# Optimization experiments

Hardware: AMD Instinct MI355X
Metric: run time of the kernel (lower is better)

Reference implementation:

```python
import jax, jax.numpy as jnp
import numpy as np

B, S, IN_DIM, LATENT, SYM = 16, 256, 512, 512, 128
NUM_NODES, NUM_CODES, MAX_OPS, MAX_BUS = 4, 512, 4, 32
HALT_EPS, MAX_SEQ = 1e-3, 256


def setup_inputs() -> dict:
    key = jax.random.key(0)
    ks = jax.random.split(key, 10)

    def lin(k, out_d, in_d, pre=()):
        kw, kb = jax.random.split(k)
        lim = 1.0 / np.sqrt(in_d).astype(np.float32)
        w = jax.random.uniform(kw, pre + (out_d, in_d), minval=-lim, maxval=lim, dtype=jnp.float32)
        b = jax.random.uniform(kb, pre + (out_d,), minval=-lim, maxval=lim, dtype=jnp.float32)
        return w, b

    x = jax.random.normal(ks[0], (B, S, IN_DIM), jnp.float32)
    ipw, ipb = lin(ks[1], LATENT, IN_DIM)
    tp = jax.random.normal(ks[2], (1, MAX_SEQ, LATENT), jnp.float32)
    N = (NUM_NODES,)
    sw, sb = lin(ks[3], SYM, LATENT, N)
    qw, qb = lin(ks[4], 1, SYM, N)
    rw, rb = lin(ks[5], LATENT, 2 * LATENT, N)
    c1w, c1b = lin(ks[6], LATENT, LATENT + SYM, N)
    c2w, c2b = lin(ks[7], LATENT, LATENT, N)
    cb = jax.random.normal(ks[8], (NUM_NODES, NUM_CODES, SYM), jnp.float32)
    return {"x": x, "input_proj_w": ipw, "input_proj_b": ipb, "token_prompts": tp,
            "sym_w": sw, "sym_b": sb, "qry_w": qw, "qry_b": qb,
            "read_w": rw, "read_b": rb, "c1_w": c1w, "c1_b": c1b,
            "c2_w": c2w, "c2_b": c2b, "codebook": cb}


def _forward(x, input_proj_w, input_proj_b, token_prompts, sym_w, sym_b, qry_w, qry_b,
             read_w, read_b, c1_w, c1_b, c2_w, c2_b, codebook):
    Bx, Sx, _ = x.shape
    N = Bx * Sx
    # input projection + positional prompts
    out = jnp.einsum('bsi,li->bsl', x, input_proj_w) + input_proj_b + token_prompts[:, :Sx, :]
    prev_out = out
    active = jnp.ones((Bx, Sx), bool)
    token_tags = jnp.zeros((Bx, Sx, SYM), x.dtype)
    # TensorBus rolling buffers ([max_bus, B, S, dim]); with default cfg the roll branch never fires
    sym_buf = jnp.zeros((MAX_BUS, Bx, Sx, SYM), x.dtype)          # slot 0 = zero tags (initial append)
    out_buf = jnp.zeros((MAX_BUS, Bx, Sx, LATENT), x.dtype).at[0].set(out)
    msg_mask = jnp.zeros((MAX_BUS,), bool).at[0].set(True)
    ptr = 1  # static python int: appends are a fixed unrolled schedule (1 + MAX_OPS*NUM_NODES <= MAX_BUS)
    slot_ids = jnp.arange(MAX_BUS)

    for t in range(MAX_OPS):
        # snapshot of active messages for this op step (get_active)
        snap_active = msg_mask & (slot_ids < ptr)                  # [MAX_BUS]
        syms_flat = sym_buf.reshape(MAX_BUS, N, SYM)
        outs_flat = out_buf.reshape(MAX_BUS, N, LATENT)
        keep_all = jnp.ones((MAX_BUS,), bool)
        for n in range(NUM_NODES):
            # relevance of each bus message per token; inactive slots masked out of argmax
            rel = jnp.einsum('tnd,d->tn', syms_flat, qry_w[n, 0]) + qry_b[n, 0]
            rel = jnp.where(snap_active[:, None], rel, jnp.asarray(-1e9, rel.dtype))
            top = jnp.argmax(rel, axis=0)                          # [N] chosen message per token
            chosen = jnp.take_along_axis(outs_flat, top[None, :, None], axis=0)[0]  # [N, LATENT]
            bus_ctx = chosen.reshape(Bx, Sx, LATENT)
            z = jnp.concatenate([out, bus_ctx], axis=-1)
            z_read = jnp.einsum('bsk,lk->bsl', z, read_w[n]) + read_b[n]
            raw_sym = jnp.einsum('bsl,dl->bsd', z_read, sym_w[n]) + sym_b[n]
            # EMA quantizer (eval): nearest codebook entry by euclidean distance
            flat = raw_sym.reshape(-1, SYM)
            cbn = codebook[n]
            d2 = (jnp.sum(flat * flat, axis=-1, keepdims=True)
                  - 2.0 * flat @ cbn.T + jnp.sum(cbn * cbn, axis=-1))
            idx = jnp.argmin(d2, axis=-1)
            quant = cbn[idx].reshape(Bx, Sx, SYM)
            h = jnp.concatenate([z_read, quant], axis=-1)
            hid = jax.nn.relu(jnp.einsum('bsk,lk->bsl', h, c1_w[n]) + c1_b[n])
            node_out = jnp.einsum('bsl,ol->bso', hid, c2_w[n]) + c2_b[n] + out
            # halting / selective update
            delta = jnp.linalg.norm(node_out - prev_out, axis=-1)
            halt = (delta < HALT_EPS) & active
            assigned = active if t > 0 else jnp.ones_like(active)
            upd = assigned & jnp.logical_not(halt)
            out = jnp.where(upd[..., None], node_out, out)
            token_tags = jnp.where(upd[..., None], quant, token_tags)
            # bus.append
            sym_buf = sym_buf.at[ptr].set(quant)
            out_buf = out_buf.at[ptr].set(node_out)
            msg_mask = msg_mask.at[ptr].set(True)
            ptr += 1
            # keep_mask: messages never selected by any token stay alive
            counts = jnp.zeros((MAX_BUS,), jnp.int32).at[top].add(1)
            keep_all = keep_all & (counts == 0)
            active = active & jnp.logical_not(halt)
            prev_out = out
        # mark_consumed: ones over valid slots ANDed with per-node keep masks at snapshot-active
        # slots (inactive/new slots get True -> faithful to the torch init_global_mask quirk)
        msg_mask = (slot_ids < ptr) & keep_all
    return out


def reference(x, input_proj_w, input_proj_b, token_prompts, sym_w, sym_b, qry_w, qry_b,
              read_w, read_b, c1_w, c1_b, c2_w, c2_b, codebook):
    return _forward(x, input_proj_w, input_proj_b, token_prompts, sym_w, sym_b, qry_w, qry_b,
                    read_w, read_b, c1_w, c1_b, c2_w, c2_b, codebook)
```

## Files before the change

### kernel.cpp

```cpp
#include <hip/hip_runtime.h>
#include <math.h>

namespace {

typedef _Float16 f16;
typedef __attribute__((ext_vector_type(8))) _Float16 f16x8;
typedef __attribute__((ext_vector_type(4))) float f32x4;

constexpr int TOK = 4096;
constexpr int DL  = 512;
constexpr int DS  = 128;
constexpr int NC  = 512;
constexpr int NSLOT = 13;

__device__ __forceinline__ float wsum(float v){
  #pragma unroll
  for(int o=32;o>0;o>>=1) v += __shfl_xor(v,o);
  return v;
}

__device__ __forceinline__ void gload16(const void* g, void* l){
  __builtin_amdgcn_global_load_lds(
      (const __attribute__((address_space(1))) unsigned int*)g,
      (__attribute__((address_space(3))) unsigned int*)l, 16, 0, 0);
}

__device__ __forceinline__ int slotb(int row, int g){
  return (((row ^ ((row>>2)&1))<<2) | (g ^ (row&3))) << 4;
}

template<int AMODE,int EPI>
__global__ __launch_bounds__(256,2) void mgemm(
    const f16* __restrict__ A1h, const f16* __restrict__ A1l,
    const f16* __restrict__ A2h, const f16* __restrict__ A2l,
    const f16* __restrict__ Bh, const f16* __restrict__ Bl,
    const float* __restrict__ bias, const float* __restrict__ res,
    float* __restrict__ Cf, f16* __restrict__ Ch, f16* __restrict__ Cl,
    f16* __restrict__ C2h, f16* __restrict__ C2l,
    float* __restrict__ scpv, int* __restrict__ scpi, int* __restrict__ idxg,
    const float* __restrict__ relc, const int* __restrict__ msg,
    int* __restrict__ cons, int pt, int node,
    int K, int K0)
{
  constexpr int SMB = 16384;
  __shared__ __align__(16) char smem[4*SMB];
  __shared__ int gsel[64];
  __shared__ float redv[4][32];
  __shared__ int   redi[4][32];
  const int tid = threadIdx.x, w = tid>>6, l = tid&63;
  const int m0 = blockIdx.x*64, n0 = blockIdx.y*64;
  const int NK = K>>5, SW = K0>>5;

  if(AMODE==1){
    if(tid<64){
      int m = m0+tid;
      float best = -1e9f; int bs = 0;
      for(int s=0;s<pt;s++){
        float v = msg[s] ? relc[(size_t)((s<<2)+node)*TOK + m] : -1e9f;
        if(v > best){ best=v; bs=s; }
      }
      gsel[tid]=bs;
      cons[bs]=1;
    }
    __syncthreads();
  }
  if(AMODE==2){
    if(tid<64){
      int m = m0+tid;
      float bv = -INFINITY; int bi = 0;
      #pragma unroll
      for(int y=0;y<8;y++){
        float v = scpv[(size_t)y*TOK + m];
        if(v > bv){ bv=v; bi=scpi[(size_t)y*TOK + m]; }
      }
      gsel[tid]=bi;
      idxg[m]=bi;
    }
    __syncthreads();
  }

  const f16* sp[4]; const f16* sp2[4]; int loff[4];
  #pragma unroll
  for(int i=0;i<4;i++){
    int c = 4*w+i;
    int isA = (c<8);
    int plane = isA ? (c>>2) : ((c-8)>>2);
    int cidx  = isA ? (c&3)  : ((c-8)&3);
    loff[i] = (isA?0:8192) + plane*4096 + cidx*1024;
    int s = (cidx<<6) + l;
    int rp = s>>2, row = rp ^ ((rp>>2)&1), g = (s&3) ^ (row&3);
    int g8 = g<<3;
    if(isA){
      int m = m0 + row;
      const f16* p1 = (plane? A1l : A1h) + ((size_t)m<<9) + g8;
      sp[i] = p1;
      if(AMODE==1)      sp2[i] = (plane? A2l : A2h) + ((size_t)gsel[row]<<21) + ((size_t)m<<9) + g8;
      else if(AMODE==2) sp2[i] = (plane? A2l : A2h) + ((size_t)gsel[row]<<7) + g8;
      else              sp2[i] = p1;
    } else {
      sp[i] = (plane? Bl : Bh) + (size_t)(n0+row)*K + g8;
      sp2[i] = sp[i];
    }
  }

  const int wr = w>>1, wc = w&1, q = l>>4, r = l&15;
  int aoff[2], boff[2];
  #pragma unroll
  for(int i=0;i<2;i++) aoff[i] = slotb(32*wr + 16*i + r, q);
  #pragma unroll
  for(int j=0;j<2;j++) boff[j] = 8192 + slotb(32*wc + 16*j + r, q);

  f32x4 acc1[2][2] = {}, acc2[2][2] = {};

  auto advance = [&](int snext){
    #pragma unroll
    for(int i=0;i<4;i++){
      if(AMODE!=0 && (4*w+i)<8 && snext==SW) sp[i] = sp2[i];
      else                                    sp[i] += 32;
    }
  };
  auto stage = [&](int buf){
    char* dst = smem + buf*SMB;
    #pragma unroll
    for(int i=0;i<4;i++) gload16(sp[i], dst + loff[i]);
  };

  f16x8 X[8], Y[8];
  auto ldfrag = [&](const char* Lb, f16x8* F){
    F[0] = *(const f16x8*)(Lb + aoff[0]);
    F[1] = *(const f16x8*)(Lb + aoff[1]);
    F[2] = *(const f16x8*)(Lb + 4096 + aoff[0]);
    F[3] = *(const f16x8*)(Lb + 4096 + aoff[1]);
    F[4] = *(const f16x8*)(Lb + boff[0]);
    F[5] = *(const f16x8*)(Lb + boff[1]);
    F[6] = *(const f16x8*)(Lb + 4096 + boff[0]);
    F[7] = *(const f16x8*)(Lb + 4096 + boff[1]);
  };
  auto domfma = [&](const f16x8* F){
    #pragma unroll
    for(int i=0;i<2;i++)
      #pragma unroll
      for(int j=0;j<2;j++){
        acc1[i][j] = __builtin_amdgcn_mfma_f32_16x16x32_f16(F[i],   F[4+j], acc1[i][j], 0,0,0);
        acc2[i][j] = __builtin_amdgcn_mfma_f32_16x16x32_f16(F[i],   F[6+j], acc2[i][j], 0,0,0);
        acc2[i][j] = __builtin_amdgcn_mfma_f32_16x16x32_f16(F[2+i], F[4+j], acc2[i][j], 0,0,0);
      }
  };

  stage(0); advance(1);
  stage(1); advance(2);
  stage(2); advance(3);
  asm volatile("s_waitcnt vmcnt(4)" ::: "memory");
  __builtin_amdgcn_s_barrier();
  ldfrag(smem, X);

  for(int kt=0; kt<NK; kt+=2){
    ldfrag(smem + ((kt+1)&3)*SMB, Y);
    if(kt+3 < NK){ stage((kt+3)&3); advance(kt+4); }
    domfma(X);
    if(kt+3 < NK)      { asm volatile("s_waitcnt vmcnt(4)" ::: "memory"); }
    else if(kt+2 < NK) { asm volatile("s_waitcnt vmcnt(0)" ::: "memory"); }
    __builtin_amdgcn_s_barrier();
    if(kt+2 < NK) ldfrag(smem + ((kt+2)&3)*SMB, X);
    if(kt+4 < NK){ stage((kt+4)&3); advance(kt+5); }
    domfma(Y);
    if(kt+4 < NK)      { asm volatile("s_waitcnt vmcnt(4)" ::: "memory"); }
    else if(kt+3 < NK) { asm volatile("s_waitcnt vmcnt(0)" ::: "memory"); }
    if(kt+2 < NK) __builtin_amdgcn_s_barrier();
  }

  if(EPI!=1){
    #pragma unroll
    for(int i=0;i<2;i++)
      #pragma unroll
      for(int j=0;j<2;j++)
        #pragma unroll
        for(int rr=0;rr<4;rr++){
          int rowm = m0 + 32*wr + 16*i + 4*q + rr;
          int coln = n0 + 32*wc + 16*j + r;
          size_t o = ((size_t)rowm<<9) + coln;
          float v = acc1[i][j][rr] + acc2[i][j][rr]*(1.0f/2048.0f) + bias[coln];
          if(EPI==2) v = fmaxf(v, 0.f);
          if(EPI==3) v += res[o];
          if(EPI==4) v += res[(((size_t)(rowm&255))<<9) + coln];
          if(EPI==3 || EPI==4) Cf[o] = v;
          if(EPI==0 || EPI==2 || EPI==4){
            f16 h = (f16)v;
            Ch[o] = h; Cl[o] = (f16)((v-(float)h)*2048.0f);
          }
          if((EPI==3 || EPI==4) && C2h){
            f16 h = (f16)v;
            C2h[o] = h; C2l[o] = (f16)((v-(float)h)*2048.0f);
          }
        }
  } else {
    #pragma unroll
    for(int i=0;i<2;i++)
      #pragma unroll
      for(int rr=0;rr<4;rr++){
        float v0 = acc1[i][0][rr] + acc2[i][0][rr]*(1.0f/2048.0f) + bias[n0+32*wc+r];
        float v1 = acc1[i][1][rr] + acc2[i][1][rr]*(1.0f/2048.0f) + bias[n0+32*wc+16+r];
        float bv; int bc;
        if(v1 > v0){ bv=v1; bc=n0+32*wc+16+r; } else { bv=v0; bc=n0+32*wc+r; }
        #pragma unroll
        for(int o=1;o<16;o<<=1){
          float ov = __shfl_xor(bv,o); int oi = __shfl_xor(bc,o);
          if(ov>bv || (ov==bv && oi<bc)){ bv=ov; bc=oi; }
        }
        if(r==0){ redv[w][16*i+4*q+rr]=bv; redi[w][16*i+4*q+rr]=bc; }
      }
    __syncthreads();
    if(tid<64){
      int wr2 = tid>>5, li = tid&31;
      float bv = redv[2*wr2][li]; int bc = redi[2*wr2][li];
      float ov = redv[2*wr2+1][li]; int oi = redi[2*wr2+1][li];
      if(ov>bv || (ov==bv && oi<bc)){ bv=ov; bc=oi; }
      scpv[(size_t)blockIdx.y*TOK + m0 + tid] = bv;
      scpi[(size_t)blockIdx.y*TOK + m0 + tid] = bc;
    }
  }
}

__global__ void split_k(const float* __restrict__ src, f16* __restrict__ hi,
                        f16* __restrict__ lo, int n){
  for(int i = blockIdx.x*256 + threadIdx.x; i < n; i += gridDim.x*256){
    float v = src[i];
    f16 h = (f16)v;
    hi[i] = h;
    lo[i] = (f16)((v - (float)h)*2048.0f);
  }
}

struct SplitArg { const float* src; f16* hi; f16* lo; int n; };
struct SplitArgs5 { SplitArg a[5]; };
__global__ void splitm_k(SplitArgs5 A){
  int stride = gridDim.x*256;
  #pragma unroll
  for(int s=0;s<5;s++){
    const float* src = A.a[s].src; f16* hi = A.a[s].hi; f16* lo = A.a[s].lo;
    int n = A.a[s].n;
    for(int i = blockIdx.x*256 + threadIdx.x; i < n; i += stride){
      float v = src[i];
      f16 h = (f16)v;
      hi[i] = h;
      lo[i] = (f16)((v - (float)h)*2048.0f);
    }
  }
}

__global__ __launch_bounds__(256)
void wcomb_k(const float* __restrict__ A, const float* __restrict__ Wall,
             float* __restrict__ C)
{
  constexpr int T=256;
  __shared__ float As[32][68];
  __shared__ float Ws[32][132];
  const int tid = threadIdx.x;
  const int m0 = blockIdx.x*64, n0 = blockIdx.y*128;
  const float* W = Wall + (size_t)(m0>>9)*DS*DL;
  const int ty = tid>>4, tx = tid&15;
  float4 pa[2], pw[4];
  auto loadA = [&](int k0){
    #pragma unroll
    for(int it=0; it<2; ++it){
      int v = tid + T*it; int rr = v>>3, c4 = v&7;
      pa[it] = *(const float4*)(A + (size_t)(m0+rr)*DS + k0 + (c4<<2));
    }
  };
  auto loadW = [&](int k0){
    #pragma unroll
    for(int it=0; it<4; ++it){
      int v = tid + T*it; int rr = v>>5, c4 = v&31;
      pw[it] = *(const float4*)(W + (size_t)(k0+rr)*DL + n0 + (c4<<2));
    }
  };
  float acc[4][8];
  #pragma unroll
  for(int i=0;i<4;i++)
    #pragma unroll
    for(int j=0;j<8;j++) acc[i][j]=0.f;
  loadA(0); loadW(0);
  for(int k0=0; k0<DS; k0+=32){
    __syncthreads();
    #pragma unroll
    for(int it=0; it<2; ++it){
      int v = tid + T*it; int rr=v>>3, c4=v&7;
      As[(c4<<2)+0][rr]=pa[it].x; As[(c4<<2)+1][rr]=pa[it].y;
      As[(c4<<2)+2][rr]=pa[it].z; As[(c4<<2)+3][rr]=pa[it].w;
    }
    #pragma unroll
    for(int it=0; it<4; ++it){
      int v = tid + T*it; int rr=v>>5, c4=v&31;
      *(float4*)&Ws[rr][c4<<2] = pw[it];
    }
    __syncthreads();
    if(k0+32 < DS){ loadA(k0+32); loadW(k0+32); }
    #pragma unroll
    for(int kk=0; kk<32; kk++){
      float4 a4 = *(const float4*)&As[kk][ty<<2];
      float4 b0 = *(const float4*)&Ws[kk][tx<<2];
      float4 b1 = *(const float4*)&Ws[kk][64+(tx<<2)];
      float a[4]={a4.x,a4.y,a4.z,a4.w};
      float b[8]={b0.x,b0.y,b0.z,b0.w,b1.x,b1.y,b1.z,b1.w};
      #pragma unroll
      for(int i=0;i<4;i++)
        #pragma unroll
        for(int j=0;j<8;j++) acc[i][j] = fmaf(a[i], b[j], acc[i][j]);
    }
  }
  #pragma unroll
  for(int i=0;i<4;i++){
    int m = m0 + (ty<<2) + i;
    #pragma unroll
    for(int j=0;j<8;j++){
      int n = n0 + ((j<4)? (tx<<2)+j : 64+(tx<<2)+(j-4));
      C[((size_t)m<<9)+n] = acc[i][j];
    }
  }
}

__global__ void init_k(int* __restrict__ msg, int* __restrict__ act,
                       float* __restrict__ relc, const float* __restrict__ qb,
                       int* __restrict__ cons){
  int i = blockIdx.x*256 + threadIdx.x;
  if(i < TOK){
    act[i] = 1;
    #pragma unroll
    for(int nn=0;nn<4;nn++) relc[nn*TOK + i] = qb[nn];
  }
  if(i < 32){ msg[i] = (i==0) ? 1 : 0; cons[i] = 0; }
}

__global__ void bias2_k(const float* __restrict__ cb, const float* __restrict__ sb,
                        float* __restrict__ b2){
  int row = blockIdx.x*4 + (threadIdx.x>>6);
  int lane = threadIdx.x&63;
  const float* cv = cb + ((size_t)row<<7);
  const float* sbn = sb + ((row>>9)<<7);
  float c0=cv[lane], c1=cv[lane+64];
  float nrm = c0*c0 + c1*c1;
  float dt  = c0*sbn[lane] + c1*sbn[lane+64];
  nrm = wsum(nrm); dt = wsum(dt);
  if(lane==0) b2[row] = dt - 0.5f*nrm;
}

__global__ void mupdate_k(const float* __restrict__ no_, float* __restrict__ out,
                          f16* __restrict__ outh, f16* __restrict__ outl,
                          float* __restrict__ relc, const int* __restrict__ idx,
                          const float* __restrict__ cbn, const float* __restrict__ qw,
                          const float* __restrict__ qb, int* __restrict__ act,
                          int* __restrict__ cons, int* __restrict__ msg,
                          int t, int ptr, int pe){
  int m = blockIdx.x*4 + (threadIdx.x>>6);
  int lane = threadIdx.x&63;
  const float* nrow = no_ + ((size_t)m<<9);
  float* orow = out + ((size_t)m<<9);
  float nv[8]; float s=0.f;
  #pragma unroll
  for(int rr=0;rr<8;rr++){
    int c = lane + (rr<<6);
    nv[rr]=nrow[c];
    float d = nv[rr]-orow[c]; s += d*d;
  }
  s = wsum(s);
  float delta = sqrtf(s);
  int a = act[m];
  int halt = (delta < 1e-3f) && a;
  int assigned = (t>0) ? a : 1;
  int upd = assigned && !halt;
  if(lane==0) act[m] = a && !halt;
  if(upd){
    #pragma unroll
    for(int rr=0;rr<8;rr++){
      int c = lane + (rr<<6);
      float v = nv[rr];
      orow[c] = v;
      f16 h = (f16)v;
      outh[((size_t)m<<9)+c] = h;
      outl[((size_t)m<<9)+c] = (f16)((v-(float)h)*2048.0f);
    }
  }
  if(ptr >= 0){
    const float* qv = cbn + ((size_t)idx[m]<<7);
    float q0=qv[lane], q1=qv[lane+64];
    #pragma unroll
    for(int nn=0;nn<4;nn++){
      float pr = q0*qw[(nn<<7)+lane] + q1*qw[(nn<<7)+64+lane];
      pr = wsum(pr);
      if(lane==0) relc[(size_t)((ptr<<2)+nn)*TOK + m] = pr + qb[nn];
    }
  }
  if(pe >= 0 && blockIdx.x==0 && threadIdx.x < 32){
    int s2 = threadIdx.x;
    msg[s2] = (s2 < pe) && !cons[s2];
    cons[s2] = 0;
  }
}

}

extern "C" void kernel_launch(void* const* d_in, const int* in_sizes, int n_in,
                              void* d_out, int out_size, void* d_ws, size_t ws_size,
                              hipStream_t stream)
{
  (void)in_sizes; (void)n_in; (void)out_size; (void)ws_size;
  const float* x   = (const float*)d_in[0];
  const float* ipw = (const float*)d_in[1];
  const float* ipb = (const float*)d_in[2];
  const float* tp  = (const float*)d_in[3];
  const float* sw  = (const float*)d_in[4];
  const float* sb  = (const float*)d_in[5];
  const float* qw  = (const float*)d_in[6];
  const float* qb  = (const float*)d_in[7];
  const float* rw  = (const float*)d_in[8];
  const float* rb  = (const float*)d_in[9];
  const float* c1w = (const float*)d_in[10];
  const float* c1b = (const float*)d_in[11];
  const float* c2w = (const float*)d_in[12];
  const float* c2b = (const float*)d_in[13];
  const float* cb  = (const float*)d_in[14];
  float* out = (float*)d_out;

  char* p = (char*)d_ws;
  auto alloc = [&](size_t b)->char*{ char* r=p; p += (b+255)&~(size_t)255; return r; };
  f16* slabh = (f16*)alloc((size_t)NSLOT*TOK*DL*2);
  f16* slabl = (f16*)alloc((size_t)NSLOT*TOK*DL*2);
  f16* outh  = (f16*)alloc((size_t)TOK*DL*2);
  f16* outl  = (f16*)alloc((size_t)TOK*DL*2);
  f16* zh    = (f16*)alloc((size_t)TOK*DL*2);
  f16* zl    = (f16*)alloc((size_t)TOK*DL*2);
  f16* hh    = (f16*)alloc((size_t)TOK*DL*2);
  f16* hl    = (f16*)alloc((size_t)TOK*DL*2);
  float* sn  = (float*)alloc((size_t)TOK*DL*4);
  f16* rwh   = (f16*)alloc((size_t)4*DL*1024*2);
  f16* rwl   = (f16*)alloc((size_t)4*DL*1024*2);
  f16* c1h   = (f16*)alloc((size_t)4*DL*640*2);
  f16* c1l   = (f16*)alloc((size_t)4*DL*640*2);
  f16* c2h   = (f16*)alloc((size_t)4*DL*DL*2);
  f16* c2l   = (f16*)alloc((size_t)4*DL*DL*2);
  f16* wch   = (f16*)alloc((size_t)4*NC*DL*2);
  f16* wcl   = (f16*)alloc((size_t)4*NC*DL*2);
  f16* iph   = (f16*)alloc((size_t)DL*DL*2);
  f16* ipl   = (f16*)alloc((size_t)DL*DL*2);
  f16* cbh   = (f16*)alloc((size_t)4*NC*DS*2);
  f16* cbl   = (f16*)alloc((size_t)4*NC*DS*2);
  float* b2  = (float*)alloc(4*NC*4);
  float* relc= (float*)alloc((size_t)NSLOT*4*TOK*4);
  float* scpv= (float*)alloc((size_t)8*TOK*4);
  int* scpi  = (int*)alloc((size_t)8*TOK*4);
  int* idxb  = (int*)alloc(TOK*4);
  int* act   = (int*)alloc(TOK*4);
  int* msg   = (int*)alloc(256);
  int* cons  = (int*)alloc(256);

  dim3 G(64,8), B(256);

  init_k<<<16,256,0,stream>>>(msg, act, relc, qb, cons);
  bias2_k<<<512,256,0,stream>>>(cb, sb, b2);
  wcomb_k<<<dim3(32,4),B,0,stream>>>(cb, sw, sn);
  split_k<<<2048,256,0,stream>>>(x, hh, hl, TOK*DL);
  SplitArgs5 sa;
  sa.a[0] = { ipw, iph, ipl, DL*DL };
  sa.a[1] = { rw,  rwh, rwl, 4*DL*1024 };
  sa.a[2] = { c1w, c1h, c1l, 4*DL*640 };
  sa.a[3] = { c2w, c2h, c2l, 4*DL*DL };
  sa.a[4] = { cb,  cbh, cbl, 4*NC*DS };
  splitm_k<<<2048,256,0,stream>>>(sa);
  split_k<<<1024,256,0,stream>>>(sn, wch, wcl, 4*NC*DL);

  mgemm<0,4><<<G,B,0,stream>>>(hh,hl, nullptr,nullptr, iph,ipl,
      ipb, tp, out, outh,outl, slabh,slabl,
      nullptr,nullptr,nullptr, nullptr,nullptr,nullptr, 0,0, DL, DL);

  int ptr = 1;
  for(int t=0;t<4;t++){
    int pt = 1 + 4*t;
    for(int n=0;n<4;n++){
      mgemm<1,0><<<G,B,0,stream>>>(outh,outl, slabh,slabl,
          rwh+(size_t)n*DL*1024, rwl+(size_t)n*DL*1024, rb+(size_t)n*DL,
          nullptr, nullptr, zh,zl, nullptr,nullptr,
          nullptr,nullptr,nullptr, relc, msg, cons, pt, n, 1024, 512);
      mgemm<0,1><<<G,B,0,stream>>>(zh,zl, nullptr,nullptr,
          wch+(size_t)n*NC*DL, wcl+(size_t)n*NC*DL, b2+(size_t)n*NC,
          nullptr, nullptr, nullptr,nullptr, nullptr,nullptr,
          scpv,scpi,nullptr, nullptr,nullptr,nullptr, 0,0, 512, 512);
      mgemm<2,2><<<G,B,0,stream>>>(zh,zl, cbh+(size_t)n*NC*DS, cbl+(size_t)n*NC*DS,
          c1h+(size_t)n*DL*640, c1l+(size_t)n*DL*640, c1b+(size_t)n*DL,
          nullptr, nullptr, hh,hl, nullptr,nullptr,
          scpv,scpi,idxb, nullptr,nullptr,nullptr, 0,0, 640, 512);
      f16* sph = (t<3) ? slabh + ((size_t)ptr<<21) : nullptr;
      f16* spl = (t<3) ? slabl + ((size_t)ptr<<21) : nullptr;
      mgemm<0,3><<<G,B,0,stream>>>(hh,hl, nullptr,nullptr,
          c2h+(size_t)n*DL*DL, c2l+(size_t)n*DL*DL, c2b+(size_t)n*DL,
          out, sn, nullptr,nullptr, sph,spl,
          nullptr,nullptr,nullptr, nullptr,nullptr,nullptr, 0,0, 512, 512);
      mupdate_k<<<1024,256,0,stream>>>(sn, out, outh,outl, relc, idxb,
          cb+(size_t)n*NC*DS, qw, qb, act, cons, msg, t,
          (t<3)? ptr : -1, (n==3 && t<3)? (1+4*(t+1)) : -1);
      ptr++;
    }
  }
}
```

Baseline: 1.318 ms.

## Load B fragments directly from global into registers, shrink LDS pipeline to three stages

The GEMM kernel no longer stages the B (weight) tile through LDS. Each wave loads its B fragments straight from global memory into registers, one k-step ahead. Only A goes through a triple-buffered LDS ring, which replaces the four-stage ring and halves the per-stage size. This cuts LDS traffic and footprint and may raise occupancy, but B reads are now uncoalesced per-lane global loads that each wave repeats, and the prefetch depth drops.

```diff
diff --git a/kernel.cpp b/kernel.cpp
--- a/kernel.cpp
+++ b/kernel.cpp
@@ -42,8 +42,8 @@
     int* __restrict__ cons, int pt, int node,
     int K, int K0)
 {
-  constexpr int SMB = 16384;
-  __shared__ __align__(16) char smem[4*SMB];
+  constexpr int SMB = 8192;
+  __shared__ __align__(16) char smem[3*SMB];
   __shared__ int gsel[64];
   __shared__ float redv[4][32];
   __shared__ int   redi[4][32];
@@ -79,94 +79,102 @@
     __syncthreads();
   }
 
-  const f16* sp[4]; const f16* sp2[4]; int loff[4];
-  #pragma unroll
-  for(int i=0;i<4;i++){
-    int c = 4*w+i;
-    int isA = (c<8);
-    int plane = isA ? (c>>2) : ((c-8)>>2);
-    int cidx  = isA ? (c&3)  : ((c-8)&3);
-    loff[i] = (isA?0:8192) + plane*4096 + cidx*1024;
+  const f16* sp[2]; const f16* sp2[2]; int loff[2];
+  #pragma unroll
+  for(int i=0;i<2;i++){
+    int c = 2*w+i;
+    int plane = c>>2, cidx = c&3;
+    loff[i] = plane*4096 + cidx*1024;
     int s = (cidx<<6) + l;
     int rp = s>>2, row = rp ^ ((rp>>2)&1), g = (s&3) ^ (row&3);
     int g8 = g<<3;
-    if(isA){
-      int m = m0 + row;
-      const f16* p1 = (plane? A1l : A1h) + ((size_t)m<<9) + g8;
-      sp[i] = p1;
-      if(AMODE==1)      sp2[i] = (plane? A2l : A2h) + ((size_t)gsel[row]<<21) + ((size_t)m<<9) + g8;
-      else if(AMODE==2) sp2[i] = (plane? A2l : A2h) + ((size_t)gsel[row]<<7) + g8;
-      else              sp2[i] = p1;
-    } else {
-      sp[i] = (plane? Bl : Bh) + (size_t)(n0+row)*K + g8;
-      sp2[i] = sp[i];
-    }
+    int m = m0 + row;
+    const f16* p1 = (plane? A1l : A1h) + ((size_t)m<<9) + g8;
+    sp[i] = p1;
+    if(AMODE==1)      sp2[i] = (plane? A2l : A2h) + ((size_t)gsel[row]<<21) + ((size_t)m<<9) + g8;
+    else if(AMODE==2) sp2[i] = (plane? A2l : A2h) + ((size_t)gsel[row]<<7) + g8;
+    else              sp2[i] = p1;
   }
 
   const int wr = w>>1, wc = w&1, q = l>>4, r = l&15;
-  int aoff[2], boff[2];
+  int aoff[2];
   #pragma unroll
   for(int i=0;i<2;i++) aoff[i] = slotb(32*wr + 16*i + r, q);
-  #pragma unroll
-  for(int j=0;j<2;j++) boff[j] = 8192 + slotb(32*wc + 16*j + r, q);
+
+  const f16* pB0h = Bh + (size_t)(n0 + 32*wc      + r)*K + (q<<3);
+  const f16* pB1h = Bh + (size_t)(n0 + 32*wc + 16 + r)*K + (q<<3);
+  const f16* pB0l = Bl + (size_t)(n0 + 32*wc      + r)*K + (q<<3);
+  const f16* pB1l = Bl + (size_t)(n0 + 32*wc + 16 + r)*K + (q<<3);
 
   f32x4 acc1[2][2] = {}, acc2[2][2] = {};
+  f16x8 BX[4], BY[4], FA[4];
 
   auto advance = [&](int snext){
     #pragma unroll
-    for(int i=0;i<4;i++){
-      if(AMODE!=0 && (4*w+i)<8 && snext==SW) sp[i] = sp2[i];
-      else                                    sp[i] += 32;
+    for(int i=0;i<2;i++){
+      if(AMODE!=0 && snext==SW) sp[i] = sp2[i];
+      else                      sp[i] += 32;
     }
   };
   auto stage = [&](int buf){
     char* dst = smem + buf*SMB;
     #pragma unroll
-    for(int i=0;i<4;i++) gload16(sp[i], dst + loff[i]);
-  };
-
-  f16x8 X[8], Y[8];
-  auto ldfrag = [&](const char* Lb, f16x8* F){
-    F[0] = *(const f16x8*)(Lb + aoff[0]);
-    F[1] = *(const f16x8*)(Lb + aoff[1]);
-    F[2] = *(const f16x8*)(Lb + 4096 + aoff[0]);
-    F[3] = *(const f16x8*)(Lb + 4096 + aoff[1]);
-    F[4] = *(const f16x8*)(Lb + boff[0]);
-    F[5] = *(const f16x8*)(Lb + boff[1]);
-    F[6] = *(const f16x8*)(Lb + 4096 + boff[0]);
-    F[7] = *(const f16x8*)(Lb + 4096 + boff[1]);
-  };
-  auto domfma = [&](const f16x8* F){
+    for(int i=0;i<2;i++) gload16(sp[i], dst + loff[i]);
+  };
+  auto loadB = [&](f16x8* D, int kt){
+    size_t o = (size_t)kt*32;
+    D[0] = *(const f16x8*)(pB0h + o);
+    D[1] = *(const f16x8*)(pB1h + o);
+    D[2] = *(const f16x8*)(pB0l + o);
+    D[3] = *(const f16x8*)(pB1l + o);
+  };
+  auto ldfragA = [&](const char* Lb){
+    FA[0] = *(const f16x8*)(Lb + aoff[0]);
+    FA[1] = *(const f16x8*)(Lb + aoff[1]);
+    FA[2] = *(const f16x8*)(Lb + 4096 + aoff[0]);
+    FA[3] = *(const f16x8*)(Lb + 4096 + aoff[1]);
+  };
+  auto domfma = [&](const f16x8* Bv){
     #pragma unroll
     for(int i=0;i<2;i++)
       #pragma unroll
       for(int j=0;j<2;j++){
-        acc1[i][j] = __builtin_amdgcn_mfma_f32_16x16x32_f16(F[i],   F[4+j], acc1[i][j], 0,0,0);
-        acc2[i][j] = __builtin_amdgcn_mfma_f32_16x16x32_f16(F[i],   F[6+j], acc2[i][j], 0,0,0);
-        acc2[i][j] = __builtin_amdgcn_mfma_f32_16x16x32_f16(F[2+i], F[4+j], acc2[i][j], 0,0,0);
+        acc1[i][j] = __builtin_amdgcn_mfma_f32_16x16x32_f16(FA[i],   Bv[j],   acc1[i][j], 0,0,0);
+        acc2[i][j] = __builtin_amdgcn_mfma_f32_16x16x32_f16(FA[i],   Bv[2+j], acc2[i][j], 0,0,0);
+        acc2[i][j] = __builtin_amdgcn_mfma_f32_16x16x32_f16(FA[2+i], Bv[j],   acc2[i][j], 0,0,0);
       }
   };
 
   stage(0); advance(1);
   stage(1); advance(2);
-  stage(2); advance(3);
-  asm volatile("s_waitcnt vmcnt(4)" ::: "memory");
+  loadB(BX, 0);
+  asm volatile("s_waitcnt vmcnt(0)" ::: "memory");
   __builtin_amdgcn_s_barrier();
-  ldfrag(smem, X);
-
+
+  int rb = 0;
   for(int kt=0; kt<NK; kt+=2){
-    ldfrag(smem + ((kt+1)&3)*SMB, Y);
-    if(kt+3 < NK){ stage((kt+3)&3); advance(kt+4); }
-    domfma(X);
-    if(kt+3 < NK)      { asm volatile("s_waitcnt vmcnt(4)" ::: "memory"); }
+    loadB(BY, kt+1);
+    if(kt+2 < NK){
+      int sb = rb+2; if(sb>=3) sb-=3;
+      stage(sb); advance(kt+3);
+    }
+    ldfragA(smem + rb*SMB);
+    domfma(BX);
+    if(kt+2 < NK){ asm volatile("s_waitcnt vmcnt(2)" ::: "memory"); }
+    else         { asm volatile("s_waitcnt vmcnt(0)" ::: "memory"); }
+    __builtin_amdgcn_s_barrier();
+    rb = (rb==2)? 0 : rb+1;
+    if(kt+2 < NK) loadB(BX, kt+2);
+    if(kt+3 < NK){
+      int sb = rb+2; if(sb>=3) sb-=3;
+      stage(sb); advance(kt+4);
+    }
+    ldfragA(smem + rb*SMB);
+    domfma(BY);
+    if(kt+3 < NK)      { asm volatile("s_waitcnt vmcnt(2)" ::: "memory"); }
     else if(kt+2 < NK) { asm volatile("s_waitcnt vmcnt(0)" ::: "memory"); }
-    __builtin_amdgcn_s_barrier();
-    if(kt+2 < NK) ldfrag(smem + ((kt+2)&3)*SMB, X);
-    if(kt+4 < NK){ stage((kt+4)&3); advance(kt+5); }
-    domfma(Y);
-    if(kt+4 < NK)      { asm volatile("s_waitcnt vmcnt(4)" ::: "memory"); }
-    else if(kt+3 < NK) { asm volatile("s_waitcnt vmcnt(0)" ::: "memory"); }
     if(kt+2 < NK) __builtin_amdgcn_s_barrier();
+    rb = (rb==2)? 0 : rb+1;
   }
 
   if(EPI!=1){
```

After: 2.024 ms. 1.54x slower.
